# Kernel tuning notes

Measured on AMD Instinct MI355X. Metric: run time of the kernel, lower is better.

Reference implementation:

```python
import jax, jax.numpy as jnp
import numpy as np

MARGIN = 0.3
BIG = 1e6  # matches the 1000000.0 additive mask in the torch code


def setup_inputs() -> dict:
    key = jax.random.key(0)
    k1, k2 = jax.random.split(key)
    embeddings = jax.random.normal(k1, (4096, 512), dtype=jnp.float32)
    labels = jax.random.randint(k2, (4096,), 0, 512)
    return {"embeddings": embeddings, "labels": labels}


def reference(embeddings, labels):
    # Pairwise euclidean distances (torch.cdist p=2) via the GEMM identity,
    # clamped before sqrt for numerical safety on the zero diagonal.
    sq = jnp.sum(embeddings * embeddings, axis=1)                      # [N]
    d2 = sq[:, None] + sq[None, :] - 2.0 * (embeddings @ embeddings.T)  # [N, N]
    dist = jnp.sqrt(jnp.maximum(d2, 1e-12))

    pos_mask = labels[None, :] == labels[:, None]   # [N, N] bool
    neg_mask = ~pos_mask

    # Hardest positive per anchor (self-distance 0 is harmless under max).
    hp = jnp.max(dist * pos_mask.astype(dist.dtype), axis=1)           # [N]

    # Semi-hard negatives: hp < d(a, n) < hp + margin, different label.
    semi_hard = (dist > hp[:, None]) & (dist < hp[:, None] + MARGIN) & neg_mask
    has_semi_hard = jnp.sum(semi_hard) > 0

    # Fallback: hardest (farthest) negative; semi-hard branch: closest semi-hard.
    hn_fallback = jnp.max(dist * neg_mask.astype(dist.dtype), axis=1)
    hn_semi = jnp.min(dist + (1.0 - semi_hard.astype(dist.dtype)) * BIG, axis=1)
    hn = jnp.where(has_semi_hard, hn_semi, hn_fallback)                # [N]

    triplet = jax.nn.relu(hp - hn + MARGIN)                            # [N]
    num_valid = jnp.sum((triplet > 0).astype(triplet.dtype))
    loss = jnp.where(num_valid > 0,
                     jnp.sum(triplet) / jnp.maximum(num_valid, 1.0),
                     jnp.mean(triplet))
    return loss
```

## Files before the change

kernel.cpp:

```cpp
#include <hip/hip_runtime.h>
#include <math.h>


constexpr float MARGIN = 0.3f;

typedef _Float16 half8    __attribute__((ext_vector_type(8)));
typedef float    floatx16 __attribute__((ext_vector_type(16)));

#define GLD_LDS16(gp, lp)                                                              \
    __builtin_amdgcn_global_load_lds(                                                  \
        (const __attribute__((address_space(1))) void*)(gp),                           \
        (__attribute__((address_space(3))) void*)(lp), 16, 0, 0)

__global__ __launch_bounds__(256)
void prep_kernel(const float* __restrict__ e, _Float16* __restrict__ pan,
                 float* __restrict__ sq, unsigned int* __restrict__ hp,
                 unsigned int* __restrict__ hn_fall, unsigned int* __restrict__ hn_semi,
                 unsigned int* __restrict__ bars, int N, int D) {
    __shared__ float red[256];
    if (blockIdx.x == 0 && threadIdx.x < 32) bars[threadIdx.x * 32] = 0u;
    const int r0  = blockIdx.x * 8;
    const int p   = r0 >> 7;
    const int rl  = r0 & 127;
    const int r   = threadIdx.x & 7;
    const int c8  = threadIdx.x >> 3;
    const int row = r0 + r;
    const float* er = e + (size_t)row * D;
    float s = 0.f;
    #pragma unroll
    for (int it = 0; it < 2; ++it) {
        const int kw = c8 + it * 32;
        const float4 x0 = *(const float4*)&er[kw * 8];
        const float4 x1 = *(const float4*)&er[kw * 8 + 4];
        const float xv[8] = {x0.x, x0.y, x0.z, x0.w, x1.x, x1.y, x1.z, x1.w};
        half8 hi, lo;
        #pragma unroll
        for (int j = 0; j < 8; ++j) {
            _Float16 h = (_Float16)xv[j];
            hi[j] = h;
            lo[j] = (_Float16)(xv[j] - (float)h);
            s += xv[j] * xv[j];
        }
        *(half8*)&pan[((size_t)(p * 128 + kw) * 128 + rl + r) * 8]      = hi;
        *(half8*)&pan[((size_t)(p * 128 + 64 + kw) * 128 + rl + r) * 8] = lo;
    }
    red[threadIdx.x] = s;
    __syncthreads();
    if (threadIdx.x < 8) {
        float t = 0.f;
        #pragma unroll
        for (int c = 0; c < 32; ++c) t += red[threadIdx.x + 8 * c];
        const int rw = r0 + threadIdx.x;
        sq[rw]      = t;
        hp[rw]      = 0u;
        hn_fall[rw] = 0u;
        hn_semi[rw] = 0x7f800000u;
    }
}

__global__ __launch_bounds__(512, 4)
void fused_kernel(const _Float16* __restrict__ pan, const int* __restrict__ labels,
                  const float* __restrict__ sq,
                  unsigned int* __restrict__ hp,
                  unsigned int* __restrict__ hn_fall,
                  unsigned int* __restrict__ hn_semi,
                  unsigned int* __restrict__ bars,
                  float* __restrict__ out,
                  int N, int D, unsigned int nrowblocks, unsigned int nblocks) {
    __shared__ __attribute__((aligned(16))) _Float16 S[3][12288];
    __shared__ float sq_r[256], sq_c[128], hp_r[256];
    __shared__ int   lab_r[256], lab_c[128];
    __shared__ int   lastflag;

    const int tid  = threadIdx.x;
    const int lane = tid & 63;
    const int wave = tid >> 6;
    const int wr = (wave >> 1) * 64;
    const int wc = (wave & 1) * 64;
    const int mrow = lane & 31;
    const int half_id = lane >> 5;

    const int j  = blockIdx.x & 7;
    const int i  = blockIdx.x >> 3;
    const int px = (j & 3) * 8 + (i & 7);
    const int py = (j >> 2) * 8 + (i >> 3);
    const int rowBase = py * 256;
    const int colBase = px * 128;

    if (tid < 256) {
        sq_r[tid]  = sq[rowBase + tid];
        lab_r[tid] = labels[rowBase + tid];
    } else if (tid < 384) {
        const int t = tid - 256;
        sq_c[t]  = sq[colBase + t];
        lab_c[t] = labels[colBase + t];
    }

    floatx16 acc[2][2];
    #pragma unroll
    for (int a = 0; a < 2; ++a)
        #pragma unroll
        for (int b = 0; b < 2; ++b)
            #pragma unroll
            for (int r = 0; r < 16; ++r) acc[a][b][r] = 0.f;

    auto stage = [&](int bufid, int kkv) {
        #pragma unroll
        for (int t = 0; t < 3; ++t) {
            const int s = wave * 3 + t;
            int kcl, p, row0, lofs;
            if (s < 16) {
                const int rq = s & 3;
                kcl  = s >> 2;
                p    = 2 * py + (rq >> 1);
                row0 = (rq & 1) * 64;
                lofs = (kcl * 256 + rq * 64) * 8;
            } else {
                const int u = s - 16;
                kcl  = u >> 1;
                p    = px;
                row0 = (u & 1) * 64;
                lofs = 8192 + (kcl * 128 + row0) * 8;
            }
            const int kc = (kcl < 2) ? (2 * kkv + kcl) : (64 + 2 * kkv + (kcl - 2));
            const _Float16* g = pan + ((size_t)(p * 128 + kc) * 128 + row0 + lane) * 8;
            GLD_LDS16(g, &S[bufid][lofs]);
        }
    };

    stage(0, 0);
    stage(1, 1);
    asm volatile("s_waitcnt vmcnt(3)" ::: "memory");
    __builtin_amdgcn_s_barrier();
    asm volatile("" ::: "memory");

    int b = 0;
    #pragma unroll 1
    for (int kk = 0; kk < 32; ++kk) {
        const int rA = wr + mrow, cB = wc + mrow;
        const _Float16* Sb = &S[b][0];
        const half8 ah0 = *(const half8*)&Sb[(half_id * 256 + rA) * 8];
        const half8 ah1 = *(const half8*)&Sb[(half_id * 256 + rA + 32) * 8];
        const half8 al0 = *(const half8*)&Sb[((2 + half_id) * 256 + rA) * 8];
        const half8 al1 = *(const half8*)&Sb[((2 + half_id) * 256 + rA + 32) * 8];
        const half8 bh0 = *(const half8*)&Sb[8192 + (half_id * 128 + cB) * 8];
        const half8 bh1 = *(const half8*)&Sb[8192 + (half_id * 128 + cB + 32) * 8];
        const half8 bl0 = *(const half8*)&Sb[8192 + ((2 + half_id) * 128 + cB) * 8];
        const half8 bl1 = *(const half8*)&Sb[8192 + ((2 + half_id) * 128 + cB + 32) * 8];
        int sb = b + 2; if (sb >= 3) sb -= 3;
        if (kk + 2 < 32) stage(sb, kk + 2);
        __builtin_amdgcn_s_setprio(1);
        acc[0][0] = __builtin_amdgcn_mfma_f32_32x32x16_f16(bh0, ah0, acc[0][0], 0, 0, 0);
        acc[0][1] = __builtin_amdgcn_mfma_f32_32x32x16_f16(bh0, ah1, acc[0][1], 0, 0, 0);
        acc[1][0] = __builtin_amdgcn_mfma_f32_32x32x16_f16(bh1, ah0, acc[1][0], 0, 0, 0);
        acc[1][1] = __builtin_amdgcn_mfma_f32_32x32x16_f16(bh1, ah1, acc[1][1], 0, 0, 0);
        acc[0][0] = __builtin_amdgcn_mfma_f32_32x32x16_f16(bl0, ah0, acc[0][0], 0, 0, 0);
        acc[0][1] = __builtin_amdgcn_mfma_f32_32x32x16_f16(bl0, ah1, acc[0][1], 0, 0, 0);
        acc[1][0] = __builtin_amdgcn_mfma_f32_32x32x16_f16(bl1, ah0, acc[1][0], 0, 0, 0);
        acc[1][1] = __builtin_amdgcn_mfma_f32_32x32x16_f16(bl1, ah1, acc[1][1], 0, 0, 0);
        acc[0][0] = __builtin_amdgcn_mfma_f32_32x32x16_f16(bh0, al0, acc[0][0], 0, 0, 0);
        acc[0][1] = __builtin_amdgcn_mfma_f32_32x32x16_f16(bh0, al1, acc[0][1], 0, 0, 0);
        acc[1][0] = __builtin_amdgcn_mfma_f32_32x32x16_f16(bh1, al0, acc[1][0], 0, 0, 0);
        acc[1][1] = __builtin_amdgcn_mfma_f32_32x32x16_f16(bh1, al1, acc[1][1], 0, 0, 0);
        __builtin_amdgcn_s_setprio(0);
        if (kk < 30) { asm volatile("s_waitcnt vmcnt(3)" ::: "memory"); }
        else         { asm volatile("s_waitcnt vmcnt(0)" ::: "memory"); }
        __builtin_amdgcn_s_barrier();
        asm volatile("" ::: "memory");
        b = (b == 2) ? 0 : b + 1;
    }

    float sqr[2]; int labr[2];
    #pragma unroll
    for (int ai = 0; ai < 2; ++ai) {
        sqr[ai]  = sq_r[wr + ai * 32 + mrow];
        labr[ai] = lab_r[wr + ai * 32 + mrow];
    }

    #pragma unroll
    for (int ai = 0; ai < 2; ++ai) {
        float vp = 0.f, vn = 0.f;
        #pragma unroll
        for (int bj = 0; bj < 2; ++bj) {
            #pragma unroll
            for (int r = 0; r < 16; ++r) {
                const int c = wc + bj * 32 + (r & 3) + 8 * (r >> 2) + 4 * half_id;
                float d = sqrtf(fmaxf(sqr[ai] + sq_c[c] - 2.0f * acc[bj][ai][r], 1e-12f));
                const bool pos = (labr[ai] == lab_c[c]);
                vp = fmaxf(vp, pos ? d : 0.f);
                vn = fmaxf(vn, pos ? 0.f : d);
            }
        }
        vp = fmaxf(vp, __shfl_xor(vp, 32, 64));
        vn = fmaxf(vn, __shfl_xor(vn, 32, 64));
        if (half_id == 0) {
            atomicMax(&hp[rowBase + wr + ai * 32 + mrow],      __float_as_uint(vp));
            atomicMax(&hn_fall[rowBase + wr + ai * 32 + mrow], __float_as_uint(vn));
        }
    }

    __syncthreads();
    unsigned int* ctr = &bars[py * 32];
    if (tid == 0) {
        __threadfence();
        atomicAdd(ctr, 1u);
        while (__hip_atomic_load(ctr, __ATOMIC_ACQUIRE, __HIP_MEMORY_SCOPE_AGENT)
               < nrowblocks)
            __builtin_amdgcn_s_sleep(32);
    }
    __syncthreads();
    if (tid < 256)
        hp_r[tid] = __uint_as_float(__hip_atomic_load(&hp[rowBase + tid],
                                    __ATOMIC_RELAXED, __HIP_MEMORY_SCOPE_AGENT));
    __syncthreads();

    #pragma unroll
    for (int ai = 0; ai < 2; ++ai) {
        const float hpv = hp_r[wr + ai * 32 + mrow];
        float vm = __builtin_inff();
        #pragma unroll
        for (int bj = 0; bj < 2; ++bj) {
            #pragma unroll
            for (int r = 0; r < 16; ++r) {
                const int c = wc + bj * 32 + (r & 3) + 8 * (r >> 2) + 4 * half_id;
                float d = sqrtf(fmaxf(sqr[ai] + sq_c[c] - 2.0f * acc[bj][ai][r], 1e-12f));
                const bool cand = (labr[ai] != lab_c[c]) && (d > hpv);
                vm = fminf(vm, cand ? d : __builtin_inff());
            }
        }
        vm = fminf(vm, __shfl_xor(vm, 32, 64));
        if (half_id == 0)
            atomicMin(&hn_semi[rowBase + wr + ai * 32 + mrow], __float_as_uint(vm));
    }

    __syncthreads();
    if (tid == 0) {
        __threadfence();
        unsigned int old = atomicAdd(&bars[992], 1u);
        lastflag = (old == nblocks - 1) ? 1 : 0;
    }
    __syncthreads();
    if (!lastflag) return;
    if (tid == 0) __threadfence();
    __syncthreads();

    float* FS = (float*)&S[0][0];
    int*   IC = (int*)(FS + 512);
    int*   IA = IC + 512;
    int any = 0;
    for (int r = tid; r < N; r += 512) {
        float h  = __uint_as_float(__hip_atomic_load(&hp[r],      __ATOMIC_RELAXED, __HIP_MEMORY_SCOPE_AGENT));
        float hs = __uint_as_float(__hip_atomic_load(&hn_semi[r], __ATOMIC_RELAXED, __HIP_MEMORY_SCOPE_AGENT));
        any |= (hs < h + MARGIN) ? 1 : 0;
    }
    IA[tid] = any;
    __syncthreads();
    for (int s = 256; s; s >>= 1) {
        if (tid < s) IA[tid] |= IA[tid + s];
        __syncthreads();
    }
    const bool has_semi = IA[0] != 0;
    float sum = 0.f; int valid = 0;
    for (int r = tid; r < N; r += 512) {
        float h  = __uint_as_float(__hip_atomic_load(&hp[r], __ATOMIC_RELAXED, __HIP_MEMORY_SCOPE_AGENT));
        float hn = has_semi
            ? __uint_as_float(__hip_atomic_load(&hn_semi[r], __ATOMIC_RELAXED, __HIP_MEMORY_SCOPE_AGENT))
            : __uint_as_float(__hip_atomic_load(&hn_fall[r], __ATOMIC_RELAXED, __HIP_MEMORY_SCOPE_AGENT));
        float t = fmaxf(h - hn + MARGIN, 0.f);
        if (!(t > 0.f)) t = 0.f;
        sum += t;
        valid += (t > 0.f) ? 1 : 0;
    }
    FS[tid] = sum; IC[tid] = valid;
    __syncthreads();
    for (int s = 256; s; s >>= 1) {
        if (tid < s) { FS[tid] += FS[tid + s]; IC[tid] += IC[tid + s]; }
        __syncthreads();
    }
    if (tid == 0) {
        float total = FS[0]; int v = IC[0];
        out[0] = (v > 0) ? (total / (float)v) : (total / (float)N);
    }
}

extern "C" void kernel_launch(void* const* d_in, const int* in_sizes, int n_in,
                              void* d_out, int out_size, void* d_ws, size_t ws_size,
                              hipStream_t stream) {
    const float* e      = (const float*)d_in[0];
    const int*   labels = (const int*)d_in[1];
    const int N = in_sizes[1];
    const int D = in_sizes[0] / N;
    float* out = (float*)d_out;

    float*        sq      = (float*)d_ws;
    unsigned int* hp      = (unsigned int*)d_ws + N;
    unsigned int* hn_fall = hp + N;
    unsigned int* hn_semi = hn_fall + N;
    unsigned int* bars    = hn_semi + N;

    const size_t small_bytes = ((size_t)(4 * N + 1024) * 4 + 255) & ~(size_t)255;
    _Float16* pan = (_Float16*)((char*)d_ws + small_bytes);

    prep_kernel<<<N / 8, 256, 0, stream>>>(e, pan, sq, hp, hn_fall, hn_semi, bars, N, D);

    const int ntx = N / 128, nty = N / 256;
    fused_kernel<<<ntx * nty, 512, 0, stream>>>(pan, labels, sq, hp, hn_fall, hn_semi,
                                                bars, out, N, D,
                                                (unsigned)ntx, (unsigned)(ntx * nty));
}
```

Measured before the change: 149.3 us.

## Enlarge fused GEMM tile to 256x256 with double-buffered deeper K slabs

Grows the per-block output tile from 256x128 to 256x256, so each wave computes 128x64 with 8 accumulators, and halves the grid to 256 blocks. The K-step loaded into LDS per stage doubles (4 hi and 4 lo chunks) with two buffers instead of three, and loads are interleaved across four compute phases split by barriers. The aim is more MFMA work per LDS byte and fewer redundant global loads of the column panel. In exchange it lowers occupancy (launch bounds 2, about 128KB LDS), adds more barriers per iteration, and leaves a 256-block grid that gives only one block per CU on a 256-CU part. That grid size also matters for the spin-barrier, which needs all blocks of a row group resident at once.

```diff
diff --git a/kernel.cpp b/kernel.cpp
--- a/kernel.cpp
+++ b/kernel.cpp
@@ -35,11 +35,11 @@
         const float xv[8] = {x0.x, x0.y, x0.z, x0.w, x1.x, x1.y, x1.z, x1.w};
         half8 hi, lo;
         #pragma unroll
-        for (int j = 0; j < 8; ++j) {
-            _Float16 h = (_Float16)xv[j];
-            hi[j] = h;
-            lo[j] = (_Float16)(xv[j] - (float)h);
-            s += xv[j] * xv[j];
+        for (int jj = 0; jj < 8; ++jj) {
+            _Float16 h = (_Float16)xv[jj];
+            hi[jj] = h;
+            lo[jj] = (_Float16)(xv[jj] - (float)h);
+            s += xv[jj] * xv[jj];
         }
         *(half8*)&pan[((size_t)(p * 128 + kw) * 128 + rl + r) * 8]      = hi;
         *(half8*)&pan[((size_t)(p * 128 + 64 + kw) * 128 + rl + r) * 8] = lo;
@@ -58,7 +58,7 @@
     }
 }
 
-__global__ __launch_bounds__(512, 4)
+__global__ __launch_bounds__(512, 2)
 void fused_kernel(const _Float16* __restrict__ pan, const int* __restrict__ labels,
                   const float* __restrict__ sq,
                   unsigned int* __restrict__ hp,
@@ -67,124 +67,137 @@
                   unsigned int* __restrict__ bars,
                   float* __restrict__ out,
                   int N, int D, unsigned int nrowblocks, unsigned int nblocks) {
-    __shared__ __attribute__((aligned(16))) _Float16 S[3][12288];
-    __shared__ float sq_r[256], sq_c[128], hp_r[256];
-    __shared__ int   lab_r[256], lab_c[128];
+    __shared__ __attribute__((aligned(16))) _Float16 S[2][32768];
+    __shared__ float sq_r[256], sq_c[256], hp_r[256];
+    __shared__ int   lab_r[256], lab_c[256];
     __shared__ int   lastflag;
 
     const int tid  = threadIdx.x;
     const int lane = tid & 63;
     const int wave = tid >> 6;
-    const int wr = (wave >> 1) * 64;
-    const int wc = (wave & 1) * 64;
+    const int wr   = (wave >> 2) * 128;
+    const int wcol = (wave & 3) * 64;
     const int mrow = lane & 31;
     const int half_id = lane >> 5;
 
     const int j  = blockIdx.x & 7;
     const int i  = blockIdx.x >> 3;
-    const int px = (j & 3) * 8 + (i & 7);
-    const int py = (j >> 2) * 8 + (i >> 3);
+    const int px = (j & 3) * 4 + (i & 3);
+    const int py = (j >> 2) * 8 + (i >> 2);
     const int rowBase = py * 256;
-    const int colBase = px * 128;
+    const int colBase = px * 256;
 
     if (tid < 256) {
         sq_r[tid]  = sq[rowBase + tid];
         lab_r[tid] = labels[rowBase + tid];
-    } else if (tid < 384) {
-        const int t = tid - 256;
-        sq_c[t]  = sq[colBase + t];
-        lab_c[t] = labels[colBase + t];
-    }
-
-    floatx16 acc[2][2];
-    #pragma unroll
-    for (int a = 0; a < 2; ++a)
-        #pragma unroll
-        for (int b = 0; b < 2; ++b)
-            #pragma unroll
-            for (int r = 0; r < 16; ++r) acc[a][b][r] = 0.f;
-
-    auto stage = [&](int bufid, int kkv) {
-        #pragma unroll
-        for (int t = 0; t < 3; ++t) {
-            const int s = wave * 3 + t;
-            int kcl, p, row0, lofs;
-            if (s < 16) {
-                const int rq = s & 3;
-                kcl  = s >> 2;
-                p    = 2 * py + (rq >> 1);
-                row0 = (rq & 1) * 64;
-                lofs = (kcl * 256 + rq * 64) * 8;
+    } else {
+        const int t2 = tid - 256;
+        sq_c[t2]  = sq[colBase + t2];
+        lab_c[t2] = labels[colBase + t2];
+    }
+
+    floatx16 acc[2][4];
+    #pragma unroll
+    for (int b = 0; b < 2; ++b)
+        #pragma unroll
+        for (int a = 0; a < 4; ++a)
+            #pragma unroll
+            for (int r = 0; r < 16; ++r) acc[b][a][r] = 0.f;
+
+    auto stage_slab = [&](int nxt, int t, int u) {
+        const int s = wave * 8 + u;
+        int kcl, pp, rowin, lofs;
+        if (s < 32) {
+            kcl = s >> 2; const int rq = s & 3;
+            pp    = 2 * py + (rq >> 1);
+            rowin = (rq & 1) * 64 + lane;
+            lofs  = (kcl * 256 + rq * 64) * 8;
+        } else {
+            const int u2 = s - 32;
+            kcl = u2 >> 2; const int cq = u2 & 3;
+            pp    = 2 * px + (cq >> 1);
+            rowin = (cq & 1) * 64 + lane;
+            lofs  = 16384 + (kcl * 256 + cq * 64) * 8;
+        }
+        const int kc = (kcl < 4) ? (4 * t + kcl) : (64 + 4 * t + (kcl - 4));
+        const _Float16* g = pan + ((size_t)(pp * 128 + kc) * 128 + rowin) * 8;
+        GLD_LDS16(g, &S[nxt][lofs]);
+    };
+
+    #pragma unroll
+    for (int u = 0; u < 8; ++u) stage_slab(0, 0, u);
+    __syncthreads();
+
+    #pragma unroll 1
+    for (int t = 0; t < 16; ++t) {
+        const int cur = t & 1, nxt = cur ^ 1;
+        const _Float16* Sc = &S[cur][0];
+        half8 ah[4], bh[2];
+        #pragma unroll
+        for (int ph = 0; ph < 4; ++ph) {
+            const int kbase = (ph >> 1) * 2 + (ph & 1) * 4;
+            half8 av[4], bv[2];
+            #pragma unroll
+            for (int ai = 0; ai < 4; ++ai)
+                av[ai] = *(const half8*)&Sc[((kbase + half_id) * 256 + wr + ai * 32 + mrow) * 8];
+            #pragma unroll
+            for (int bj = 0; bj < 2; ++bj)
+                bv[bj] = *(const half8*)&Sc[16384 + ((kbase + half_id) * 256 + wcol + bj * 32 + mrow) * 8];
+            if (t + 1 < 16) {
+                stage_slab(nxt, t + 1, 2 * ph);
+                stage_slab(nxt, t + 1, 2 * ph + 1);
+            }
+            asm volatile("" ::: "memory");
+            __builtin_amdgcn_s_barrier();
+            asm volatile("" ::: "memory");
+            __builtin_amdgcn_s_setprio(1);
+            if ((ph & 1) == 0) {
+                #pragma unroll
+                for (int bj = 0; bj < 2; ++bj)
+                    #pragma unroll
+                    for (int ai = 0; ai < 4; ++ai)
+                        acc[bj][ai] = __builtin_amdgcn_mfma_f32_32x32x16_f16(
+                            bv[bj], av[ai], acc[bj][ai], 0, 0, 0);
+                #pragma unroll
+                for (int ai = 0; ai < 4; ++ai) ah[ai] = av[ai];
+                bh[0] = bv[0]; bh[1] = bv[1];
             } else {
-                const int u = s - 16;
-                kcl  = u >> 1;
-                p    = px;
-                row0 = (u & 1) * 64;
-                lofs = 8192 + (kcl * 128 + row0) * 8;
+                #pragma unroll
+                for (int bj = 0; bj < 2; ++bj)
+                    #pragma unroll
+                    for (int ai = 0; ai < 4; ++ai)
+                        acc[bj][ai] = __builtin_amdgcn_mfma_f32_32x32x16_f16(
+                            bh[bj], av[ai], acc[bj][ai], 0, 0, 0);
+                #pragma unroll
+                for (int bj = 0; bj < 2; ++bj)
+                    #pragma unroll
+                    for (int ai = 0; ai < 4; ++ai)
+                        acc[bj][ai] = __builtin_amdgcn_mfma_f32_32x32x16_f16(
+                            bv[bj], ah[ai], acc[bj][ai], 0, 0, 0);
             }
-            const int kc = (kcl < 2) ? (2 * kkv + kcl) : (64 + 2 * kkv + (kcl - 2));
-            const _Float16* g = pan + ((size_t)(p * 128 + kc) * 128 + row0 + lane) * 8;
-            GLD_LDS16(g, &S[bufid][lofs]);
-        }
-    };
-
-    stage(0, 0);
-    stage(1, 1);
-    asm volatile("s_waitcnt vmcnt(3)" ::: "memory");
-    __builtin_amdgcn_s_barrier();
-    asm volatile("" ::: "memory");
-
-    int b = 0;
-    #pragma unroll 1
-    for (int kk = 0; kk < 32; ++kk) {
-        const int rA = wr + mrow, cB = wc + mrow;
-        const _Float16* Sb = &S[b][0];
-        const half8 ah0 = *(const half8*)&Sb[(half_id * 256 + rA) * 8];
-        const half8 ah1 = *(const half8*)&Sb[(half_id * 256 + rA + 32) * 8];
-        const half8 al0 = *(const half8*)&Sb[((2 + half_id) * 256 + rA) * 8];
-        const half8 al1 = *(const half8*)&Sb[((2 + half_id) * 256 + rA + 32) * 8];
-        const half8 bh0 = *(const half8*)&Sb[8192 + (half_id * 128 + cB) * 8];
-        const half8 bh1 = *(const half8*)&Sb[8192 + (half_id * 128 + cB + 32) * 8];
-        const half8 bl0 = *(const half8*)&Sb[8192 + ((2 + half_id) * 128 + cB) * 8];
-        const half8 bl1 = *(const half8*)&Sb[8192 + ((2 + half_id) * 128 + cB + 32) * 8];
-        int sb = b + 2; if (sb >= 3) sb -= 3;
-        if (kk + 2 < 32) stage(sb, kk + 2);
-        __builtin_amdgcn_s_setprio(1);
-        acc[0][0] = __builtin_amdgcn_mfma_f32_32x32x16_f16(bh0, ah0, acc[0][0], 0, 0, 0);
-        acc[0][1] = __builtin_amdgcn_mfma_f32_32x32x16_f16(bh0, ah1, acc[0][1], 0, 0, 0);
-        acc[1][0] = __builtin_amdgcn_mfma_f32_32x32x16_f16(bh1, ah0, acc[1][0], 0, 0, 0);
-        acc[1][1] = __builtin_amdgcn_mfma_f32_32x32x16_f16(bh1, ah1, acc[1][1], 0, 0, 0);
-        acc[0][0] = __builtin_amdgcn_mfma_f32_32x32x16_f16(bl0, ah0, acc[0][0], 0, 0, 0);
-        acc[0][1] = __builtin_amdgcn_mfma_f32_32x32x16_f16(bl0, ah1, acc[0][1], 0, 0, 0);
-        acc[1][0] = __builtin_amdgcn_mfma_f32_32x32x16_f16(bl1, ah0, acc[1][0], 0, 0, 0);
-        acc[1][1] = __builtin_amdgcn_mfma_f32_32x32x16_f16(bl1, ah1, acc[1][1], 0, 0, 0);
-        acc[0][0] = __builtin_amdgcn_mfma_f32_32x32x16_f16(bh0, al0, acc[0][0], 0, 0, 0);
-        acc[0][1] = __builtin_amdgcn_mfma_f32_32x32x16_f16(bh0, al1, acc[0][1], 0, 0, 0);
-        acc[1][0] = __builtin_amdgcn_mfma_f32_32x32x16_f16(bh1, al0, acc[1][0], 0, 0, 0);
-        acc[1][1] = __builtin_amdgcn_mfma_f32_32x32x16_f16(bh1, al1, acc[1][1], 0, 0, 0);
-        __builtin_amdgcn_s_setprio(0);
-        if (kk < 30) { asm volatile("s_waitcnt vmcnt(3)" ::: "memory"); }
-        else         { asm volatile("s_waitcnt vmcnt(0)" ::: "memory"); }
-        __builtin_amdgcn_s_barrier();
-        asm volatile("" ::: "memory");
-        b = (b == 2) ? 0 : b + 1;
-    }
-
-    float sqr[2]; int labr[2];
-    #pragma unroll
-    for (int ai = 0; ai < 2; ++ai) {
+            __builtin_amdgcn_s_setprio(0);
+            if (ph == 3) { asm volatile("s_waitcnt vmcnt(0)" ::: "memory"); }
+            asm volatile("" ::: "memory");
+            __builtin_amdgcn_s_barrier();
+            asm volatile("" ::: "memory");
+        }
+    }
+
+    float sqr[4]; int labr[4];
+    #pragma unroll
+    for (int ai = 0; ai < 4; ++ai) {
         sqr[ai]  = sq_r[wr + ai * 32 + mrow];
         labr[ai] = lab_r[wr + ai * 32 + mrow];
     }
 
     #pragma unroll
-    for (int ai = 0; ai < 2; ++ai) {
+    for (int ai = 0; ai < 4; ++ai) {
         float vp = 0.f, vn = 0.f;
         #pragma unroll
         for (int bj = 0; bj < 2; ++bj) {
             #pragma unroll
             for (int r = 0; r < 16; ++r) {
-                const int c = wc + bj * 32 + (r & 3) + 8 * (r >> 2) + 4 * half_id;
+                const int c = wcol + bj * 32 + (r & 3) + 8 * (r >> 2) + 4 * half_id;
                 float d = sqrtf(fmaxf(sqr[ai] + sq_c[c] - 2.0f * acc[bj][ai][r], 1e-12f));
                 const bool pos = (labr[ai] == lab_c[c]);
                 vp = fmaxf(vp, pos ? d : 0.f);
@@ -215,14 +228,14 @@
     __syncthreads();
 
     #pragma unroll
-    for (int ai = 0; ai < 2; ++ai) {
+    for (int ai = 0; ai < 4; ++ai) {
         const float hpv = hp_r[wr + ai * 32 + mrow];
         float vm = __builtin_inff();
         #pragma unroll
         for (int bj = 0; bj < 2; ++bj) {
             #pragma unroll
             for (int r = 0; r < 16; ++r) {
-                const int c = wc + bj * 32 + (r & 3) + 8 * (r >> 2) + 4 * half_id;
+                const int c = wcol + bj * 32 + (r & 3) + 8 * (r >> 2) + 4 * half_id;
                 float d = sqrtf(fmaxf(sqr[ai] + sq_c[c] - 2.0f * acc[bj][ai][r], 1e-12f));
                 const bool cand = (labr[ai] != lab_c[c]) && (d > hpv);
                 vm = fminf(vm, cand ? d : __builtin_inff());
@@ -303,7 +316,7 @@
 
     prep_kernel<<<N / 8, 256, 0, stream>>>(e, pan, sq, hp, hn_fall, hn_semi, bars, N, D);
 
-    const int ntx = N / 128, nty = N / 256;
+    const int ntx = N / 256, nty = N / 256;
     fused_kernel<<<ntx * nty, 512, 0, stream>>>(pan, labels, sq, hp, hn_fall, hn_semi,
                                                 bars, out, N, D,
                                                 (unsigned)ntx, (unsigned)(ntx * nty));
```

Result: faster. 140.1 us (-6.2%).
